# Kernel optimization log

Measured on AMD Instinct MI355X. Metric: run time of the kernel, lower is better.

Reference implementation:

```python
import jax, jax.numpy as jnp
import numpy as np

INPUT_DIM = 512
OUTPUT_DIM = 512
DEGREE = 7
ALPHA = 0.5


def setup_inputs() -> dict:
    key = jax.random.key(0)
    kx, kc = jax.random.split(key)
    x = jax.random.normal(kx, (8192, INPUT_DIM), dtype=jnp.float32)
    std = 1.0 / (INPUT_DIM * (DEGREE + 1))
    laguerre_coeffs = jax.random.normal(kc, (INPUT_DIM, OUTPUT_DIM, DEGREE + 1), dtype=jnp.float32) * std
    return {"x": x, "laguerre_coeffs": laguerre_coeffs}


def reference(x, laguerre_coeffs):
    # x: [B, I] -> tanh squashed
    xt = jnp.tanh(x.reshape(-1, INPUT_DIM))
    # Build Laguerre basis L_0..L_degree via the standard recurrence:
    # k*L_k = (2(k-1)+1+alpha - x)*L_{k-1} - (k-1+alpha)*L_{k-2}
    L0 = jnp.ones_like(xt)
    basis = [L0]
    if DEGREE > 0:
        L1 = 1.0 + ALPHA - xt
        basis.append(L1)
        Lkm2, Lkm1 = L0, L1
        for k in range(2, DEGREE + 1):
            Lk = ((2 * (k - 1) + 1 + ALPHA - xt) * Lkm1 - (k - 1 + ALPHA) * Lkm2) / k
            basis.append(Lk)
            Lkm2, Lkm1 = Lkm1, Lk
    laguerre = jnp.stack(basis, axis=-1)  # [B, I, D+1]
    y = jnp.einsum('bid,iod->bo', laguerre, laguerre_coeffs)
    return y
```

## Files before the change

### kernel.cpp

```cpp
#include <hip/hip_runtime.h>

#define B_ROWS 8192
#define IN_DIM 512
#define OUT_DIM 512
#define NDEG 8
#define KDIM (IN_DIM * NDEG)
#define ZSLICES 4
#define NKT 16

typedef short bf16x8 __attribute__((ext_vector_type(8)));
typedef float f32x4  __attribute__((ext_vector_type(4)));

__device__ __forceinline__ unsigned short f2bf(float f) {
  unsigned u = __float_as_uint(f);
  u += 0x7fffu + ((u >> 16) & 1u);
  return (unsigned short)(u >> 16);
}

__device__ __forceinline__ void laguerre8(float t, float* L) {
  L[0] = 1.0f;
  L[1] = 1.5f - t;
#pragma unroll
  for (int k = 2; k < NDEG; ++k)
    L[k] = ((2.0f * (float)k - 0.5f - t) * L[k - 1] -
            ((float)k - 0.5f) * L[k - 2]) * (1.0f / (float)k);
}

__device__ __forceinline__ float ftanh(float x) {
  float e2 = __expf(2.0f * x);
  return (e2 - 1.0f) * (1.0f / (e2 + 1.0f));
}

__device__ __forceinline__ uint4 bpack(float xv) {
  float L[NDEG];
  laguerre8(ftanh(xv), L);
  uint4 v;
  v.x = (unsigned)f2bf(L[0]) | ((unsigned)f2bf(L[1]) << 16);
  v.y = (unsigned)f2bf(L[2]) | ((unsigned)f2bf(L[3]) << 16);
  v.z = (unsigned)f2bf(L[4]) | ((unsigned)f2bf(L[5]) << 16);
  v.w = (unsigned)f2bf(L[6]) | ((unsigned)f2bf(L[7]) << 16);
  return v;
}


__global__ void prep_kernel(const float* __restrict__ x, const float* __restrict__ cf,
                            unsigned short* __restrict__ A, unsigned short* __restrict__ Bt) {
  int g = blockIdx.x;
  if (g < (B_ROWS * IN_DIM) / 256) {
    int idx = g * 256 + threadIdx.x;
    int b = idx >> 9, i = idx & 511;
    uint4 v = bpack(x[idx]);
    int h = b >> 7, rb = b & 127, t = i >> 3, c = i & 7;
    size_t chunk = ((size_t)(h * 64 + t)) * 1024 + (rb >> 6) * 512 + (rb & 63) * 8 + (c ^ (rb & 7));
    ((uint4*)A)[chunk] = v;
  } else {
    int idx = (g - (B_ROWS * IN_DIM) / 256) * 256 + threadIdx.x;
    int i = idx >> 9, o = idx & 511;
    const float4* cp = (const float4*)(cf + (size_t)idx * 8);
    float4 c0 = cp[0], c1 = cp[1];
    uint4 v;
    v.x = (unsigned)f2bf(c0.x) | ((unsigned)f2bf(c0.y) << 16);
    v.y = (unsigned)f2bf(c0.z) | ((unsigned)f2bf(c0.w) << 16);
    v.z = (unsigned)f2bf(c1.x) | ((unsigned)f2bf(c1.y) << 16);
    v.w = (unsigned)f2bf(c1.z) | ((unsigned)f2bf(c1.w) << 16);
    int h = o >> 7, rb = o & 127, t = i >> 3, c = i & 7;
    size_t chunk = ((size_t)(h * 64 + t)) * 1024 + (rb >> 6) * 512 + (rb & 63) * 8 + (c ^ (rb & 7));
    ((uint4*)Bt)[chunk] = v;
  }
}


#define SB __builtin_amdgcn_sched_barrier(0)

#define LDA(SET, buf, mq, ks)                                                      \
  { const unsigned short* Ab_ = lds + (buf)*16384 + wm*8192 + (mq)*4096 + arow*64; \
    _Pragma("unroll") for (int m4 = 0; m4 < 4; ++m4)                               \
      SET[m4] = *(const bf16x8*)(Ab_ + m4*1024 + (e ^ ((ks)*32))); }

#define LDB_(SET, buf, ks)                                                         \
  { const unsigned short* Bb_ = lds + 32768 + (buf)*16384 + (wn>>1)*8192           \
                                + (wn&1)*4096 + arow*64;                           \
    _Pragma("unroll") for (int ni = 0; ni < 4; ++ni)                               \
      SET[ni] = *(const bf16x8*)(Bb_ + ni*1024 + (e ^ ((ks)*32))); }

#define MM(ASET, BSET, mq)                                                         \
  { __builtin_amdgcn_s_setprio(1);                                                 \
    _Pragma("unroll") for (int m4 = 0; m4 < 4; ++m4)                               \
      _Pragma("unroll") for (int ni = 0; ni < 4; ++ni)                             \
        acc[(mq)*4+m4][ni] = __builtin_amdgcn_mfma_f32_16x16x32_bf16(              \
            ASET[m4], BSET[ni], acc[(mq)*4+m4][ni], 0, 0, 0);                      \
    __builtin_amdgcn_s_setprio(0); }

__global__ __launch_bounds__(512, 2) void gemm_kernel(const unsigned short* __restrict__ A,
                                                      const unsigned short* __restrict__ Bt,
                                                      unsigned short* __restrict__ P) {
  __shared__ unsigned short lds[65536];

  const int tid = threadIdx.x;
  const int lane = tid & 63;
  const int w = tid >> 6;
  const int wm = w >> 2, wn = w & 3;

  const int g = blockIdx.x;
  const int j0 = g >> 3, xx = g & 7;
  const int My = ((j0 >> 3) << 3) | xx;
  const int n = (j0 >> 2) & 1;
  const int z = j0 & 3;

  const uint4* Ag = (const uint4*)A;
  const uint4* Bg = (const uint4*)Bt;

  const int arow = lane & 15, hi = lane >> 4;
  const int e = (hi ^ (arow & 7)) * 8;

  f32x4 zero = {0.f, 0.f, 0.f, 0.f};
  f32x4 acc[8][4];
#pragma unroll
  for (int mi = 0; mi < 8; ++mi)
#pragma unroll
    for (int ni = 0; ni < 4; ++ni) acc[mi][ni] = zero;

  auto STAGE_H = [&](int isB, int h, int tile, int buf) {
    const uint4* src = isB ? Bg : Ag;
    const int rowblk = (isB ? n * 2 : My * 2) + h;
    const size_t c0 = ((size_t)(rowblk * 64 + z * NKT + tile)) * 1024 + w * 64 + lane;
    unsigned short* d = lds + isB * 32768 + buf * 16384 + h * 8192 + w * 512;
    __builtin_amdgcn_global_load_lds(
        (const __attribute__((address_space(1))) unsigned int*)(src + c0),
        (__attribute__((address_space(3))) unsigned int*)d, 16, 0, 0);
    __builtin_amdgcn_global_load_lds(
        (const __attribute__((address_space(1))) unsigned int*)(src + c0 + 512),
        (__attribute__((address_space(3))) unsigned int*)(d + 4096), 16, 0, 0);
  };

  bf16x8 afA[4], afB[4], bfA[4], bfB[4];

  STAGE_H(0, 0, 0, 0); STAGE_H(0, 1, 0, 0);
  STAGE_H(1, 0, 0, 0); STAGE_H(1, 1, 0, 0);
  STAGE_H(1, 0, 1, 1);
  asm volatile("s_waitcnt vmcnt(2)" ::: "memory");
  SB;
  __builtin_amdgcn_s_barrier();
  SB;
  LDA(afA, 0, 0, 0); LDB_(bfA, 0, 0);

  for (int it = 0; it < 7; ++it) {
    const int t1 = 2 * it + 1, t2 = 2 * it + 2, t3 = 2 * it + 3;
    LDA(afB, 0, 1, 0); STAGE_H(1, 1, t1, 1); SB; MM(afA, bfA, 0);
    LDA(afA, 0, 0, 1); LDB_(bfB, 0, 1); STAGE_H(0, 0, t1, 1); SB; MM(afB, bfA, 1);
    LDA(afB, 0, 1, 1); STAGE_H(0, 1, t1, 1); SB; MM(afA, bfB, 0);
    __builtin_amdgcn_s_barrier(); SB;
    STAGE_H(1, 0, t2, 0); SB;
    MM(afB, bfB, 1);
    asm volatile("s_waitcnt vmcnt(2)" ::: "memory"); SB;
    __builtin_amdgcn_s_barrier(); SB;
    LDA(afA, 1, 0, 0); LDB_(bfA, 1, 0);
    LDA(afB, 1, 1, 0); STAGE_H(0, 0, t2, 0); SB; MM(afA, bfA, 0);
    LDA(afA, 1, 0, 1); LDB_(bfB, 1, 1); STAGE_H(0, 1, t2, 0); SB; MM(afB, bfA, 1);
    LDA(afB, 1, 1, 1); STAGE_H(1, 1, t2, 0); SB; MM(afA, bfB, 0);
    __builtin_amdgcn_s_barrier(); SB;
    STAGE_H(1, 0, t3, 1); SB;
    MM(afB, bfB, 1);
    asm volatile("s_waitcnt vmcnt(2)" ::: "memory"); SB;
    __builtin_amdgcn_s_barrier(); SB;
    LDA(afA, 0, 0, 0); LDB_(bfA, 0, 0);
  }
  LDA(afB, 0, 1, 0); STAGE_H(1, 1, 15, 1); SB; MM(afA, bfA, 0);
  LDA(afA, 0, 0, 1); LDB_(bfB, 0, 1); STAGE_H(0, 0, 15, 1); SB; MM(afB, bfA, 1);
  LDA(afB, 0, 1, 1); STAGE_H(0, 1, 15, 1); SB; MM(afA, bfB, 0);
  MM(afB, bfB, 1);
  asm volatile("s_waitcnt vmcnt(0)" ::: "memory"); SB;
  __builtin_amdgcn_s_barrier(); SB;
  LDA(afA, 1, 0, 0); LDB_(bfA, 1, 0);
  LDA(afB, 1, 1, 0); SB; MM(afA, bfA, 0);
  LDA(afA, 1, 0, 1); LDB_(bfB, 1, 1); SB; MM(afB, bfA, 1);
  LDA(afB, 1, 1, 1); SB; MM(afA, bfB, 0);
  MM(afB, bfB, 1);
  __syncthreads();

  unsigned short* W = lds + w * 8192;
#pragma unroll
  for (int mi = 0; mi < 8; ++mi)
#pragma unroll
    for (int ni = 0; ni < 4; ++ni) {
      int col = ni * 16 + arow;
      int c8 = col >> 3, cpos = col & 7;
#pragma unroll
      for (int r = 0; r < 4; ++r) {
        int row = mi * 16 + hi * 4 + r;
        W[row * 64 + ((c8 ^ (row & 7)) << 3) + cpos] = f2bf(acc[mi][ni][r]);
      }
    }
  const int rr = lane >> 3, cc = lane & 7;
#pragma unroll
  for (int it = 0; it < 16; ++it) {
    int row = it * 8 + rr;
    uint4 v = *(uint4*)&W[row * 64 + ((cc ^ (row & 7)) << 3)];
    size_t pr = ((size_t)z * B_ROWS + My * 256 + wm * 128 + row) * 512 + n * 256 + wn * 64 + cc * 8;
    *(uint4*)&P[pr] = v;
  }
}

__global__ void reduce_kernel(const unsigned short* __restrict__ P, float* __restrict__ out) {
  size_t t = (size_t)blockIdx.x * 256 + threadIdx.x;
  const uint4* p = (const uint4*)P;
  const size_t stride = (size_t)B_ROWS * OUT_DIM / 8;
  float s[8] = {0, 0, 0, 0, 0, 0, 0, 0};
#pragma unroll
  for (int zz = 0; zz < ZSLICES; ++zz) {
    uint4 v = p[t + zz * stride];
    unsigned q[4] = {v.x, v.y, v.z, v.w};
#pragma unroll
    for (int j = 0; j < 4; ++j) {
      s[2 * j]     += __uint_as_float((q[j] & 0xffffu) << 16);
      s[2 * j + 1] += __uint_as_float(q[j] & 0xffff0000u);
    }
  }
  float4 o0 = {s[0], s[1], s[2], s[3]}, o1 = {s[4], s[5], s[6], s[7]};
  ((float4*)out)[t * 2]     = o0;
  ((float4*)out)[t * 2 + 1] = o1;
}

__global__ void naive_kernel(const float* __restrict__ x, const float* __restrict__ c,
                             float* __restrict__ out) {
  __shared__ float bas[IN_DIM * NDEG];
  int b = blockIdx.x;
  for (int i = threadIdx.x; i < IN_DIM; i += 256) {
    float t = tanhf(x[(size_t)b * IN_DIM + i]);
    float L[NDEG];
    laguerre8(t, L);
#pragma unroll
    for (int d = 0; d < NDEG; ++d) bas[i * NDEG + d] = L[d];
  }
  __syncthreads();
  for (int o = threadIdx.x; o < OUT_DIM; o += 256) {
    float acc = 0.f;
    for (int i = 0; i < IN_DIM; ++i) {
      const float* cp = c + ((size_t)i * OUT_DIM + o) * NDEG;
#pragma unroll
      for (int d = 0; d < NDEG; ++d) acc += bas[i * NDEG + d] * cp[d];
    }
    out[(size_t)b * OUT_DIM + o] = acc;
  }
}

extern "C" void kernel_launch(void* const* d_in, const int* in_sizes, int n_in,
                              void* d_out, int out_size, void* d_ws, size_t ws_size,
                              hipStream_t stream) {
  const float* x    = (const float*)d_in[0];
  const float* coef = (const float*)d_in[1];
  float* out = (float*)d_out;

  const size_t A_B  = (size_t)B_ROWS * KDIM * 2;
  const size_t P_B  = (size_t)ZSLICES * B_ROWS * OUT_DIM * 2;
  const size_t BT_B = (size_t)OUT_DIM * KDIM * 2;

  if (ws_size >= A_B + P_B + BT_B) {
    unsigned short* Abuf = (unsigned short*)d_ws;
    unsigned short* Pp   = (unsigned short*)((char*)d_ws + A_B);
    unsigned short* Bt   = (unsigned short*)((char*)d_ws + A_B + P_B);
    prep_kernel<<<(B_ROWS * IN_DIM) / 256 + (IN_DIM * OUT_DIM) / 256, 256, 0, stream>>>(x, coef, Abuf, Bt);
    gemm_kernel<<<256, 512, 0, stream>>>(Abuf, Bt, Pp);
    reduce_kernel<<<(B_ROWS * OUT_DIM / 8) / 256, 256, 0, stream>>>(Pp, out);
  } else {
    naive_kernel<<<B_ROWS, 256, 0, stream>>>(x, coef, out);
  }
}
```

Before: 66.15 us.

## Fuse Laguerre basis generation into GEMM A-operand loads from raw x

The separate materialisation of the bf16 Laguerre basis matrix A (8192x4096) is removed. The GEMM now loads raw x floats straight into registers and computes tanh, the Laguerre recurrence and bf16 packing inline, so only the coefficient matrix is staged through LDS. This drops a 64 MB write and re-read of A and halves LDS usage per stage. In exchange, each workgroup recomputes the basis for its tiles across the N blocks, adds VALU work between MFMAs, and switches to truncating rounding (add 0x8000, not round-to-nearest-even) for bf16.

```diff
diff --git a/kernel.cpp b/kernel.cpp
--- a/kernel.cpp
+++ b/kernel.cpp
@@ -11,6 +11,8 @@
 typedef short bf16x8 __attribute__((ext_vector_type(8)));
 typedef float f32x4  __attribute__((ext_vector_type(4)));
 
+#define SB __builtin_amdgcn_sched_barrier(0)
+
 __device__ __forceinline__ unsigned short f2bf(float f) {
   unsigned u = __float_as_uint(f);
   u += 0x7fffu + ((u >> 16) & 1u);
@@ -31,67 +33,64 @@
   return (e2 - 1.0f) * (1.0f / (e2 + 1.0f));
 }
 
-__device__ __forceinline__ uint4 bpack(float xv) {
+__device__ __forceinline__ bf16x8 bpack8(float xv) {
   float L[NDEG];
   laguerre8(ftanh(xv), L);
+  bf16x8 r;
+#pragma unroll
+  for (int d = 0; d < NDEG; ++d)
+    r[d] = (short)((__float_as_uint(L[d]) + 0x8000u) >> 16);
+  return r;
+}
+
+
+__global__ void prep_kernel(const float* __restrict__ cf, unsigned short* __restrict__ Bt) {
+  int idx = blockIdx.x * 256 + threadIdx.x;
+  int i = idx >> 9, o = idx & 511;
+  const float4* cp = (const float4*)(cf + (size_t)idx * 8);
+  float4 c0 = cp[0], c1 = cp[1];
   uint4 v;
-  v.x = (unsigned)f2bf(L[0]) | ((unsigned)f2bf(L[1]) << 16);
-  v.y = (unsigned)f2bf(L[2]) | ((unsigned)f2bf(L[3]) << 16);
-  v.z = (unsigned)f2bf(L[4]) | ((unsigned)f2bf(L[5]) << 16);
-  v.w = (unsigned)f2bf(L[6]) | ((unsigned)f2bf(L[7]) << 16);
-  return v;
-}
-
-
-__global__ void prep_kernel(const float* __restrict__ x, const float* __restrict__ cf,
-                            unsigned short* __restrict__ A, unsigned short* __restrict__ Bt) {
-  int g = blockIdx.x;
-  if (g < (B_ROWS * IN_DIM) / 256) {
-    int idx = g * 256 + threadIdx.x;
-    int b = idx >> 9, i = idx & 511;
-    uint4 v = bpack(x[idx]);
-    int h = b >> 7, rb = b & 127, t = i >> 3, c = i & 7;
-    size_t chunk = ((size_t)(h * 64 + t)) * 1024 + (rb >> 6) * 512 + (rb & 63) * 8 + (c ^ (rb & 7));
-    ((uint4*)A)[chunk] = v;
-  } else {
-    int idx = (g - (B_ROWS * IN_DIM) / 256) * 256 + threadIdx.x;
-    int i = idx >> 9, o = idx & 511;
-    const float4* cp = (const float4*)(cf + (size_t)idx * 8);
-    float4 c0 = cp[0], c1 = cp[1];
-    uint4 v;
-    v.x = (unsigned)f2bf(c0.x) | ((unsigned)f2bf(c0.y) << 16);
-    v.y = (unsigned)f2bf(c0.z) | ((unsigned)f2bf(c0.w) << 16);
-    v.z = (unsigned)f2bf(c1.x) | ((unsigned)f2bf(c1.y) << 16);
-    v.w = (unsigned)f2bf(c1.z) | ((unsigned)f2bf(c1.w) << 16);
-    int h = o >> 7, rb = o & 127, t = i >> 3, c = i & 7;
-    size_t chunk = ((size_t)(h * 64 + t)) * 1024 + (rb >> 6) * 512 + (rb & 63) * 8 + (c ^ (rb & 7));
-    ((uint4*)Bt)[chunk] = v;
-  }
-}
-
-
-#define SB __builtin_amdgcn_sched_barrier(0)
-
-#define LDA(SET, buf, mq, ks)                                                      \
-  { const unsigned short* Ab_ = lds + (buf)*16384 + wm*8192 + (mq)*4096 + arow*64; \
-    _Pragma("unroll") for (int m4 = 0; m4 < 4; ++m4)                               \
-      SET[m4] = *(const bf16x8*)(Ab_ + m4*1024 + (e ^ ((ks)*32))); }
-
-#define LDB_(SET, buf, ks)                                                         \
-  { const unsigned short* Bb_ = lds + 32768 + (buf)*16384 + (wn>>1)*8192           \
-                                + (wn&1)*4096 + arow*64;                           \
+  v.x = (unsigned)f2bf(c0.x) | ((unsigned)f2bf(c0.y) << 16);
+  v.y = (unsigned)f2bf(c0.z) | ((unsigned)f2bf(c0.w) << 16);
+  v.z = (unsigned)f2bf(c1.x) | ((unsigned)f2bf(c1.y) << 16);
+  v.w = (unsigned)f2bf(c1.z) | ((unsigned)f2bf(c1.w) << 16);
+  int h = o >> 7, rb = o & 127, t = i >> 3, c = i & 7;
+  size_t chunk = ((size_t)(h * 64 + t)) * 1024 + (rb >> 6) * 512 + (rb & 63) * 8 + (c ^ (rb & 7));
+  ((uint4*)Bt)[chunk] = v;
+}
+
+
+#define LDB_(SET, cur, ks)                                                         \
+  { const unsigned short* Bb_ = lds + (cur) * 16384 + (wn >> 1) * 8192             \
+                                + (wn & 1) * 4096 + arow * 64;                     \
     _Pragma("unroll") for (int ni = 0; ni < 4; ++ni)                               \
-      SET[ni] = *(const bf16x8*)(Bb_ + ni*1024 + (e ^ ((ks)*32))); }
+      SET[ni] = *(const bf16x8*)(Bb_ + ni * 1024 + (e ^ ((ks) * 32))); }
+
+#define XL(dst, tt, mq, ks)                                                        \
+  { _Pragma("unroll") for (int m4 = 0; m4 < 4; ++m4)                               \
+      dst[m4] = xb[((mq) * 64 + m4 * 16) * 512 + (tt) * 8 + (ks) * 4]; }
+
+#define BP(dst, src)                                                               \
+  { _Pragma("unroll") for (int m4 = 0; m4 < 4; ++m4) dst[m4] = bpack8(src[m4]); }
 
 #define MM(ASET, BSET, mq)                                                         \
   { __builtin_amdgcn_s_setprio(1);                                                 \
     _Pragma("unroll") for (int m4 = 0; m4 < 4; ++m4)                               \
       _Pragma("unroll") for (int ni = 0; ni < 4; ++ni)                             \
-        acc[(mq)*4+m4][ni] = __builtin_amdgcn_mfma_f32_16x16x32_bf16(              \
-            ASET[m4], BSET[ni], acc[(mq)*4+m4][ni], 0, 0, 0);                      \
+        acc[(mq) * 4 + m4][ni] = __builtin_amdgcn_mfma_f32_16x16x32_bf16(          \
+            ASET[m4], BSET[ni], acc[(mq) * 4 + m4][ni], 0, 0, 0);                  \
     __builtin_amdgcn_s_setprio(0); }
 
-__global__ __launch_bounds__(512, 2) void gemm_kernel(const unsigned short* __restrict__ A,
+#define COMPUTE(cur, tt)                                                           \
+  { LDB_(bfA, cur, 0); XL(xq, tt, 1, 0);                                           \
+    BP(af, xp); MM(af, bfA, 0);                                                    \
+    XL(xr, tt, 0, 1);                                                              \
+    BP(af, xq); MM(af, bfA, 1);                                                    \
+    LDB_(bfB, cur, 1); XL(xq, tt, 1, 1);                                           \
+    BP(af, xr); MM(af, bfB, 0);                                                    \
+    BP(af, xq); MM(af, bfB, 1); }
+
+__global__ __launch_bounds__(512, 2) void gemm_kernel(const float* __restrict__ x,
                                                       const unsigned short* __restrict__ Bt,
                                                       unsigned short* __restrict__ P) {
   __shared__ unsigned short lds[65536];
@@ -107,12 +106,13 @@
   const int n = (j0 >> 2) & 1;
   const int z = j0 & 3;
 
-  const uint4* Ag = (const uint4*)A;
   const uint4* Bg = (const uint4*)Bt;
 
   const int arow = lane & 15, hi = lane >> 4;
   const int e = (hi ^ (arow & 7)) * 8;
 
+  const float* xb = x + ((size_t)(My * 256 + wm * 128 + arow)) * 512 + z * 128 + hi;
+
   f32x4 zero = {0.f, 0.f, 0.f, 0.f};
   f32x4 acc[8][4];
 #pragma unroll
@@ -120,62 +120,46 @@
 #pragma unroll
     for (int ni = 0; ni < 4; ++ni) acc[mi][ni] = zero;
 
-  auto STAGE_H = [&](int isB, int h, int tile, int buf) {
-    const uint4* src = isB ? Bg : Ag;
-    const int rowblk = (isB ? n * 2 : My * 2) + h;
-    const size_t c0 = ((size_t)(rowblk * 64 + z * NKT + tile)) * 1024 + w * 64 + lane;
-    unsigned short* d = lds + isB * 32768 + buf * 16384 + h * 8192 + w * 512;
-    __builtin_amdgcn_global_load_lds(
-        (const __attribute__((address_space(1))) unsigned int*)(src + c0),
-        (__attribute__((address_space(3))) unsigned int*)d, 16, 0, 0);
-    __builtin_amdgcn_global_load_lds(
-        (const __attribute__((address_space(1))) unsigned int*)(src + c0 + 512),
-        (__attribute__((address_space(3))) unsigned int*)(d + 4096), 16, 0, 0);
+  auto STAGE = [&](int tile, int buf) {
+#pragma unroll
+    for (int h = 0; h < 2; ++h) {
+      const size_t c0 = ((size_t)((n * 2 + h) * 64 + z * NKT + tile)) * 1024 + w * 64 + lane;
+      unsigned short* d = lds + buf * 16384 + h * 8192 + w * 512;
+      __builtin_amdgcn_global_load_lds(
+          (const __attribute__((address_space(1))) unsigned int*)(Bg + c0),
+          (__attribute__((address_space(3))) unsigned int*)d, 16, 0, 0);
+      __builtin_amdgcn_global_load_lds(
+          (const __attribute__((address_space(1))) unsigned int*)(Bg + c0 + 512),
+          (__attribute__((address_space(3))) unsigned int*)(d + 4096), 16, 0, 0);
+    }
   };
 
-  bf16x8 afA[4], afB[4], bfA[4], bfB[4];
-
-  STAGE_H(0, 0, 0, 0); STAGE_H(0, 1, 0, 0);
-  STAGE_H(1, 0, 0, 0); STAGE_H(1, 1, 0, 0);
-  STAGE_H(1, 0, 1, 1);
-  asm volatile("s_waitcnt vmcnt(2)" ::: "memory");
+  bf16x8 af[4], bfA[4], bfB[4];
+  float xp[4], xq[4], xr[4];
+
+  STAGE(0, 0); STAGE(1, 1);
+  XL(xp, 0, 0, 0);
+  asm volatile("s_waitcnt vmcnt(8)" ::: "memory");
   SB;
-  __builtin_amdgcn_s_barrier();
+  __builtin_amdgcn_s_barrier(); SB;
+
+#pragma unroll 2
+  for (int t = 0; t < NKT - 2; ++t) {
+    const int cur = t & 1;
+    COMPUTE(cur, t);
+    XL(xp, t + 1, 0, 0);
+    __builtin_amdgcn_s_barrier(); SB;
+    STAGE(t + 2, cur);
+    asm volatile("s_waitcnt vmcnt(8)" ::: "memory");
+    SB;
+    __builtin_amdgcn_s_barrier(); SB;
+  }
+  COMPUTE(0, 14);
+  XL(xp, 15, 0, 0);
+  asm volatile("s_waitcnt vmcnt(4)" ::: "memory");
   SB;
-  LDA(afA, 0, 0, 0); LDB_(bfA, 0, 0);
-
-  for (int it = 0; it < 7; ++it) {
-    const int t1 = 2 * it + 1, t2 = 2 * it + 2, t3 = 2 * it + 3;
-    LDA(afB, 0, 1, 0); STAGE_H(1, 1, t1, 1); SB; MM(afA, bfA, 0);
-    LDA(afA, 0, 0, 1); LDB_(bfB, 0, 1); STAGE_H(0, 0, t1, 1); SB; MM(afB, bfA, 1);
-    LDA(afB, 0, 1, 1); STAGE_H(0, 1, t1, 1); SB; MM(afA, bfB, 0);
-    __builtin_amdgcn_s_barrier(); SB;
-    STAGE_H(1, 0, t2, 0); SB;
-    MM(afB, bfB, 1);
-    asm volatile("s_waitcnt vmcnt(2)" ::: "memory"); SB;
-    __builtin_amdgcn_s_barrier(); SB;
-    LDA(afA, 1, 0, 0); LDB_(bfA, 1, 0);
-    LDA(afB, 1, 1, 0); STAGE_H(0, 0, t2, 0); SB; MM(afA, bfA, 0);
-    LDA(afA, 1, 0, 1); LDB_(bfB, 1, 1); STAGE_H(0, 1, t2, 0); SB; MM(afB, bfA, 1);
-    LDA(afB, 1, 1, 1); STAGE_H(1, 1, t2, 0); SB; MM(afA, bfB, 0);
-    __builtin_amdgcn_s_barrier(); SB;
-    STAGE_H(1, 0, t3, 1); SB;
-    MM(afB, bfB, 1);
-    asm volatile("s_waitcnt vmcnt(2)" ::: "memory"); SB;
-    __builtin_amdgcn_s_barrier(); SB;
-    LDA(afA, 0, 0, 0); LDB_(bfA, 0, 0);
-  }
-  LDA(afB, 0, 1, 0); STAGE_H(1, 1, 15, 1); SB; MM(afA, bfA, 0);
-  LDA(afA, 0, 0, 1); LDB_(bfB, 0, 1); STAGE_H(0, 0, 15, 1); SB; MM(afB, bfA, 1);
-  LDA(afB, 0, 1, 1); STAGE_H(0, 1, 15, 1); SB; MM(afA, bfB, 0);
-  MM(afB, bfB, 1);
-  asm volatile("s_waitcnt vmcnt(0)" ::: "memory"); SB;
   __builtin_amdgcn_s_barrier(); SB;
-  LDA(afA, 1, 0, 0); LDB_(bfA, 1, 0);
-  LDA(afB, 1, 1, 0); SB; MM(afA, bfA, 0);
-  LDA(afA, 1, 0, 1); LDB_(bfB, 1, 1); SB; MM(afB, bfA, 1);
-  LDA(afB, 1, 1, 1); SB; MM(afA, bfB, 0);
-  MM(afB, bfB, 1);
+  COMPUTE(1, 15);
   __syncthreads();
 
   unsigned short* W = lds + w * 8192;
@@ -226,9 +210,8 @@
   __shared__ float bas[IN_DIM * NDEG];
   int b = blockIdx.x;
   for (int i = threadIdx.x; i < IN_DIM; i += 256) {
-    float t = tanhf(x[(size_t)b * IN_DIM + i]);
     float L[NDEG];
-    laguerre8(t, L);
+    laguerre8(tanhf(x[(size_t)b * IN_DIM + i]), L);
 #pragma unroll
     for (int d = 0; d < NDEG; ++d) bas[i * NDEG + d] = L[d];
   }
@@ -251,16 +234,14 @@
   const float* coef = (const float*)d_in[1];
   float* out = (float*)d_out;
 
-  const size_t A_B  = (size_t)B_ROWS * KDIM * 2;
   const size_t P_B  = (size_t)ZSLICES * B_ROWS * OUT_DIM * 2;
   const size_t BT_B = (size_t)OUT_DIM * KDIM * 2;
 
-  if (ws_size >= A_B + P_B + BT_B) {
-    unsigned short* Abuf = (unsigned short*)d_ws;
-    unsigned short* Pp   = (unsigned short*)((char*)d_ws + A_B);
-    unsigned short* Bt   = (unsigned short*)((char*)d_ws + A_B + P_B);
-    prep_kernel<<<(B_ROWS * IN_DIM) / 256 + (IN_DIM * OUT_DIM) / 256, 256, 0, stream>>>(x, coef, Abuf, Bt);
-    gemm_kernel<<<256, 512, 0, stream>>>(Abuf, Bt, Pp);
+  if (ws_size >= P_B + BT_B) {
+    unsigned short* Pp = (unsigned short*)d_ws;
+    unsigned short* Bt = (unsigned short*)((char*)d_ws + P_B);
+    prep_kernel<<<(IN_DIM * OUT_DIM) / 256, 256, 0, stream>>>(coef, Bt);
+    gemm_kernel<<<256, 512, 0, stream>>>(x, Bt, Pp);
     reduce_kernel<<<(B_ROWS * OUT_DIM / 8) / 256, 256, 0, stream>>>(Pp, out);
   } else {
     naive_kernel<<<B_ROWS, 256, 0, stream>>>(x, coef, out);
```

Measured after the change: 98.43 us. 1.49x slower.
